# Kernel optimization log

Hardware: AMD Instinct MI355X
Metric: run time of the kernel (lower is better)

## Reference

```python
import jax, jax.numpy as jnp
import numpy as np
from jax import lax

EPS_COS = 1e-8  # torch F.cosine_similarity eps
EPS_GN = 1e-5   # torch GroupNorm eps


def setup_inputs() -> dict:
    key = jax.random.key(0)
    k1, k2, k3 = jax.random.split(key, 3)
    b, f, h, w = 4, 64, 64, 64
    fdm = jax.random.uniform(k1, (b, 1, 2 * h, 2 * w), dtype=jnp.float32)
    x = jax.random.normal(k2, (b, f, h, w), dtype=jnp.float32)
    W_fuse = jax.random.normal(k3, (f, 2 * f, 3, 3), dtype=jnp.float32) * 0.05
    b_fuse = jnp.zeros((f,), jnp.float32)
    gamma = jnp.ones((f,), jnp.float32)
    beta = jnp.zeros((f,), jnp.float32)
    return {"fdm": fdm, "x": x, "W_fuse": W_fuse, "b_fuse": b_fuse,
            "gamma": gamma, "beta": beta}


def reference(fdm, x, W_fuse, b_fuse, gamma, beta):
    b, f, h, w = x.shape
    # adaptive_max_pool2d(fdm, (h, w)): input spatial is exact multiple -> plain max pool
    kh, kw = fdm.shape[2] // h, fdm.shape[3] // w
    fdm_p = lax.reduce_window(fdm, -jnp.inf, lax.max,
                              (1, 1, kh, kw), (1, 1, kh, kw), 'VALID')  # [b,1,h,w]
    # per-sample threshold: min(0.5, max(fdm)/3)
    maxv = jnp.max(fdm_p, axis=(1, 2, 3))                 # [b]
    thre = jnp.minimum(0.5, maxv / 3.0)                   # [b]
    mask = fdm_p.reshape(b, h * w) >= thre[:, None]       # [b, HW] selected pixels

    # cosine similarity between selected feature vectors and all positions.
    # Original masked-selects N rows then computes N x HW sims and max-reduces over N;
    # we compute the full HW x HW sim and mask unselected rows to -inf (same max).
    xf = x.reshape(b, f, h * w).transpose(0, 2, 1)        # [b, HW, f]
    norm = jnp.sqrt(jnp.sum(xf * xf, axis=-1, keepdims=True))
    xn = xf / jnp.maximum(norm, EPS_COS)
    sim = jnp.einsum('bpf,bqf->bpq', xn, xn)              # [b, HW(sel), HW(all)]
    sim = jnp.where(mask[:, :, None], sim, -jnp.inf)
    sm = (jnp.max(sim, axis=1) / 2.0 + 0.5).reshape(b, 1, h, w)

    # fuse: Conv2d(2f -> f, k3, pad1) + GroupNorm(1, f) + ReLU
    cat = jnp.concatenate([sm * x, x], axis=1)            # [b, 2f, h, w]
    y = lax.conv_general_dilated(cat, W_fuse, (1, 1), 'SAME',
                                 dimension_numbers=('NCHW', 'OIHW', 'NCHW'))
    y = y + b_fuse[None, :, None, None]
    mu = jnp.mean(y, axis=(1, 2, 3), keepdims=True)
    var = jnp.mean((y - mu) ** 2, axis=(1, 2, 3), keepdims=True)
    y = (y - mu) / jnp.sqrt(var + EPS_GN)
    y = y * gamma[None, :, None, None] + beta[None, :, None, None]
    x0 = jax.nn.relu(y)
    return x0, sm
```

## Files before the change

kernel.cpp:

```cpp
#include <hip/hip_runtime.h>
#include <math.h>


#define HW 4096
#define NCH 64

typedef __attribute__((ext_vector_type(8))) short short8;
typedef __attribute__((ext_vector_type(4))) float f32x4;

static __device__ __forceinline__ ushort f2bf(float f) {
    unsigned u = __float_as_uint(f);
    unsigned r = (u + 0x7fffu + ((u >> 16) & 1u)) >> 16;
    return (ushort)r;
}
static __device__ __forceinline__ float bf2f(ushort h) {
    return __uint_as_float(((unsigned)h) << 16);
}
static __device__ __forceinline__ unsigned mapf(float f) {
    unsigned u = __float_as_uint(f);
    return u ^ ((unsigned)((int)u >> 31) | 0x80000000u);
}
static __device__ __forceinline__ float unmapf(unsigned u) {
    unsigned b = (u & 0x80000000u) ? (u ^ 0x80000000u) : ~u;
    return __uint_as_float(b);
}

__global__ __launch_bounds__(256) void k_pnp(
    const float* __restrict__ fdm, const float* __restrict__ x, const float* __restrict__ W,
    float* __restrict__ pooledOut, float* __restrict__ threOut,
    int* __restrict__ unsel, int* __restrict__ unselN, unsigned* __restrict__ scores,
    float* __restrict__ gnS1, float* __restrict__ gnS2,
    float* __restrict__ rn, float* __restrict__ smOut, ushort* __restrict__ inb,
    ushort* __restrict__ wbh, ushort* __restrict__ wbl) {
    const int t = threadIdx.x;
    if (blockIdx.x < 4) {
        const int b = blockIdx.x;
        __shared__ float pooled[4096];
        __shared__ float red[256];
        __shared__ int cnt;
        const float* fb = fdm + b * 16384;
        float lmax = -1.0f;
#pragma unroll
        for (int it = 0; it < 8; ++it) {
            int id2 = it * 256 + t;
            int i = id2 >> 5;
            int j2 = id2 & 31;
            const float* base = fb + i * 256 + j2 * 4;
            float4 a = *(const float4*)base;
            float4 c = *(const float4*)(base + 128);
            float p0 = fmaxf(fmaxf(a.x, a.y), fmaxf(c.x, c.y));
            float p1 = fmaxf(fmaxf(a.z, a.w), fmaxf(c.z, c.w));
            pooled[i * 64 + j2 * 2]     = p0;
            pooled[i * 64 + j2 * 2 + 1] = p1;
            lmax = fmaxf(lmax, fmaxf(p0, p1));
        }
        red[t] = lmax;
        __syncthreads();
        for (int s = 128; s > 0; s >>= 1) {
            if (t < s) red[t] = fmaxf(red[t], red[t + s]);
            __syncthreads();
        }
        __shared__ float thre_s;
        if (t == 0) {
            thre_s = fminf(0.5f, red[0] / 3.0f);
            cnt = 0;
            gnS1[b] = 0.0f; gnS2[b] = 0.0f;
        }
        __syncthreads();
        const float th = thre_s;
#pragma unroll
        for (int it = 0; it < 4; ++it) {
            int idx = (it * 256 + t) * 4;
            *(float4*)(pooledOut + b * 4096 + idx) = *(const float4*)(pooled + idx);
        }
        for (int idx = t; idx < 4096; idx += 256) {
            scores[b * 4096 + idx] = 0u;
            if (!(pooled[idx] >= th)) {
                int pos = atomicAdd(&cnt, 1);
                unsel[b * 4096 + pos] = idx;
            }
        }
        __syncthreads();
        if (t == 0) { unselN[b] = cnt; threOut[b] = th; }
    } else if (blockIdx.x < 260) {
        __shared__ float s_part[4][64];
        const int n = blockIdx.x - 4;
        const int b = n >> 6;
        const int pbase = (n & 63) * 64;
        const int wv = t >> 6;
        const int l = t & 63;
        const int sp = pbase + l;
        const float* xp = x + b * (NCH * HW) + sp;
        float xv[16];
        float ss = 0.f;
#pragma unroll
        for (int i = 0; i < 16; ++i) {
            float a = xp[(wv * 16 + i) * HW];
            xv[i] = a;
            ss += a * a;
        }
        s_part[wv][l] = ss;
        ushort h[16];
#pragma unroll
        for (int i = 0; i < 16; ++i) h[i] = f2bf(xv[i]);
        size_t dst1 = ((size_t)(b * 8 + wv) * 4096 + sp) * 16;
        size_t dst2 = ((size_t)(b * 8 + 4 + wv) * 4096 + sp) * 16;
        *(uint4*)(inb + dst1)     = *(const uint4*)h;
        *(uint4*)(inb + dst1 + 8) = *(const uint4*)(h + 8);
        *(uint4*)(inb + dst2)     = *(const uint4*)h;
        *(uint4*)(inb + dst2 + 8) = *(const uint4*)(h + 8);
        __syncthreads();
        if (t < 64) {
            float s = s_part[0][l] + s_part[1][l] + s_part[2][l] + s_part[3][l];
            int g = b * HW + pbase + l;
            rn[g] = 1.0f / fmaxf(sqrtf(s), 1e-8f);
            smOut[g] = 1.0f;
        }
    } else {
        const int u = (blockIdx.x - 260) * 256 + t;
        const int tap = u >> 10;
        const int rem = u & 1023;
        const int oc = rem >> 4;
        const int g = rem & 15;
        ushort hh[8], ll[8];
#pragma unroll
        for (int j = 0; j < 8; ++j) {
            int ic = g * 8 + j;
            float v = W[(oc * 128 + ic) * 9 + tap];
            ushort hb = f2bf(v);
            hh[j] = hb;
            ll[j] = f2bf(v - bf2f(hb));
        }
        *(uint4*)(wbh + (size_t)u * 8) = *(const uint4*)hh;
        *(uint4*)(wbl + (size_t)u * 8) = *(const uint4*)ll;
    }
}

__global__ __launch_bounds__(256) void k_score(
    const float* __restrict__ rn, const float* __restrict__ pooledM, const float* __restrict__ threArr,
    const int* __restrict__ unsel, const int* __restrict__ unselN,
    const ushort* __restrict__ inb, unsigned* __restrict__ scores) {
    const int b = blockIdx.y;
    const int n0 = blockIdx.x * 128;
    const int t = threadIdx.x;
    const int lane = t & 63;
    const int wave = t >> 6;
    const int li = lane & 15;
    const int quad = lane >> 4;
    const int nu = unselN[b];
    if (nu == 0) return;

    __shared__ __align__(16) ushort s_qh[64 * 72];
    __shared__ __align__(16) ushort s_ql[64 * 72];
    __shared__ unsigned s_best[64];

    const float th = threArr[b];
    const int p0 = n0 + (2 * wave) * 16 + li;
    const int p1 = n0 + (2 * wave + 1) * 16 + li;
    const float rp0 = rn[b * 4096 + p0];
    const float rp1 = rn[b * 4096 + p1];
    const float ng0 = (pooledM[b * 4096 + p0] >= th) ? 0.0f : -INFINITY;
    const float ng1 = (pooledM[b * 4096 + p1] >= th) ? 0.0f : -INFINITY;

    for (int qs0 = 0; qs0 < nu; qs0 += 64) {
        __syncthreads();
        for (int idx = t; idx < 512; idx += 256) {
            int q_l = idx >> 3;
            int part = idx & 7;
            int qg = qs0 + q_l;
            int q = 0;
            float rq = 0.0f;
            if (qg < nu) {
                q = unsel[b * 4096 + qg];
                rq = rn[b * 4096 + q];
            }
            uint4 raw = *(const uint4*)(inb + (((size_t)(b * 8 + 4 + (part >> 1)) * 4096) + q) * 16 + (part & 1) * 8);
            ushort hv[8]; *(uint4*)hv = raw;
            ushort hh[8], ll[8];
#pragma unroll
            for (int j = 0; j < 8; ++j) {
                float v = bf2f(hv[j]) * rq;
                hh[j] = f2bf(v);
                ll[j] = f2bf(v - bf2f(hh[j]));
            }
            int c0 = (part >> 1) * 16 + (part & 1) * 8;
            *(uint4*)(s_qh + q_l * 72 + c0) = *(const uint4*)hh;
            *(uint4*)(s_ql + q_l * 72 + c0) = *(const uint4*)ll;
        }
        if (t < 64) s_best[t] = 0u;
        __syncthreads();

        f32x4 acc[2][4];
#pragma unroll
        for (int nt = 0; nt < 2; ++nt)
#pragma unroll
            for (int mt = 0; mt < 4; ++mt) acc[nt][mt] = (f32x4){0.f, 0.f, 0.f, 0.f};
#pragma unroll
        for (int k0 = 0; k0 < 2; ++k0) {
            const int cb = k0 * 32 + quad * 8;
            const int grp = 4 + (cb >> 4);
            const int sub = cb & 15;
            short8 b0 = *(const short8*)(inb + (((size_t)(b * 8 + grp) * 4096) + p0) * 16 + sub);
            short8 b1 = *(const short8*)(inb + (((size_t)(b * 8 + grp) * 4096) + p1) * 16 + sub);
#pragma unroll
            for (int mt = 0; mt < 4; ++mt) {
                short8 ah = *(const short8*)(s_qh + (size_t)(mt * 16 + li) * 72 + cb);
                short8 al = *(const short8*)(s_ql + (size_t)(mt * 16 + li) * 72 + cb);
                acc[0][mt] = __builtin_amdgcn_mfma_f32_16x16x32_bf16(ah, b0, acc[0][mt], 0, 0, 0);
                acc[0][mt] = __builtin_amdgcn_mfma_f32_16x16x32_bf16(al, b0, acc[0][mt], 0, 0, 0);
                acc[1][mt] = __builtin_amdgcn_mfma_f32_16x16x32_bf16(ah, b1, acc[1][mt], 0, 0, 0);
                acc[1][mt] = __builtin_amdgcn_mfma_f32_16x16x32_bf16(al, b1, acc[1][mt], 0, 0, 0);
            }
        }
#pragma unroll
        for (int mt = 0; mt < 4; ++mt) {
#pragma unroll
            for (int r = 0; r < 4; ++r) {
                float sc = fmaxf(acc[0][mt][r] * rp0 + ng0, acc[1][mt][r] * rp1 + ng1);
                sc = fmaxf(sc, __shfl_xor(sc, 1));
                sc = fmaxf(sc, __shfl_xor(sc, 2));
                sc = fmaxf(sc, __shfl_xor(sc, 4));
                sc = fmaxf(sc, __shfl_xor(sc, 8));
                if (li == 0) atomicMax(&s_best[mt * 16 + quad * 4 + r], mapf(sc));
            }
        }
        __syncthreads();
        if (t < 64 && qs0 + t < nu) atomicMax(scores + b * 4096 + qs0 + t, s_best[t]);
    }
}

__global__ __launch_bounds__(256) void k_conv_mfma(
    const ushort* __restrict__ inb, const ushort* __restrict__ wbh, const ushort* __restrict__ wbl,
    const float* __restrict__ bfuse, const int* __restrict__ unsel, const int* __restrict__ unselN,
    const unsigned* __restrict__ scores, float* __restrict__ smOut,
    float* __restrict__ y, float* __restrict__ gnS1, float* __restrict__ gnS2) {
    const int rowblk = blockIdx.x;
    const int ocblk = blockIdx.y;
    const int b = blockIdx.z;
    const int t = threadIdx.x;
    const int lane = t & 63;
    const int wave = t >> 6;
    const int li = lane & 15;
    const int quad = lane >> 4;
    const int h0 = rowblk * 4;
    const int oc0 = ocblk * 16;
    const int nu = unselN[b];

    __shared__ __align__(16) ushort s_in[6 * 66 * 40];
    __shared__ __align__(16) ushort s_wh[9 * 16 * 40];
    __shared__ __align__(16) ushort s_wl[9 * 16 * 40];
    __shared__ float red1[256];
    __shared__ float red2[256];

    if (rowblk == 0 && ocblk == 0) {
        for (int qi = t; qi < nu; qi += 256) {
            float sm = unmapf(scores[b * 4096 + qi]) * 0.5f + 0.5f;
            smOut[b * 4096 + unsel[b * 4096 + qi]] = sm;
        }
    }

    f32x4 acc[4];
#pragma unroll
    for (int j = 0; j < 4; ++j) acc[j] = (f32x4){0.f, 0.f, 0.f, 0.f};

    for (int chunk = 0; chunk < 4; ++chunk) {
        __syncthreads();
        for (int idx = t; idx < 1584; idx += 256) {
            int part = idx & 3;
            int cell = idx >> 2;
            int r = cell / 66;
            int c = cell - r * 66;
            int h = h0 + r - 1;
            int w = c - 1;
            uint4 v = make_uint4(0u, 0u, 0u, 0u);
            if ((unsigned)h < 64u && (unsigned)w < 64u) {
                int grp = 2 * chunk + (part >> 1);
                int sub = part & 1;
                v = *(const uint4*)(inb + (((size_t)(b * 8 + grp) * 4096 + h * 64 + w) * 16 + sub * 8));
            }
            *(uint4*)(s_in + (size_t)cell * 40 + part * 8) = v;
        }
        const int ic0 = chunk * 32;
        for (int idx = t; idx < 1152; idx += 256) {
            int part = idx & 3;
            int uu = idx >> 2;
            int hl = uu / 144;
            int rem = uu - hl * 144;
            int tap = rem >> 4;
            int o = rem & 15;
            const ushort* src = (hl ? wbl : wbh) + ((size_t)(tap * 64 + oc0 + o) * 128 + ic0 + part * 8);
            uint4 v = *(const uint4*)src;
            ushort* dst = (hl ? s_wl : s_wh) + ((size_t)(tap * 16 + o) * 40 + part * 8);
            *(uint4*)dst = v;
        }
        if (chunk < 2) {
            __syncthreads();
            for (int idx = t; idx < nu * 4; idx += 256) {
                int qi = idx >> 2;
                int part = idx & 3;
                int q = unsel[b * 4096 + qi];
                int hq = q >> 6, wq = q & 63;
                int r = hq - h0 + 1;
                if ((unsigned)r < 6u) {
                    float sm = unmapf(scores[b * 4096 + qi]) * 0.5f + 0.5f;
                    ushort* ptr = s_in + (size_t)(r * 66 + wq + 1) * 40 + part * 8;
                    ushort hv[8];
                    *(uint4*)hv = *(const uint4*)ptr;
#pragma unroll
                    for (int j = 0; j < 8; ++j) hv[j] = f2bf(bf2f(hv[j]) * sm);
                    *(uint4*)ptr = *(const uint4*)hv;
                }
            }
        }
        __syncthreads();
#pragma unroll
        for (int kh = 0; kh < 3; ++kh) {
            const int r = wave + kh;
#pragma unroll
            for (int kw = 0; kw < 3; ++kw) {
                const int tap = kh * 3 + kw;
                short8 ah = *(const short8*)(s_wh + (size_t)(tap * 16 + li) * 40 + quad * 8);
                short8 al = *(const short8*)(s_wl + (size_t)(tap * 16 + li) * 40 + quad * 8);
#pragma unroll
                for (int j = 0; j < 4; ++j) {
                    int c = j * 16 + li + kw;
                    short8 bv = *(const short8*)(s_in + ((size_t)(r * 66 + c) * 40 + quad * 8));
                    acc[j] = __builtin_amdgcn_mfma_f32_16x16x32_bf16(ah, bv, acc[j], 0, 0, 0);
                    acc[j] = __builtin_amdgcn_mfma_f32_16x16x32_bf16(al, bv, acc[j], 0, 0, 0);
                }
            }
        }
    }
    float bias[4];
#pragma unroll
    for (int reg = 0; reg < 4; ++reg) bias[reg] = bfuse[oc0 + quad * 4 + reg];
    float s1 = 0.f, s2 = 0.f;
    const int hrow = h0 + wave;
#pragma unroll
    for (int j = 0; j < 4; ++j) {
#pragma unroll
        for (int reg = 0; reg < 4; ++reg) {
            float v = acc[j][reg] + bias[reg];
            y[((size_t)(b * 64 + oc0 + quad * 4 + reg)) * HW + hrow * 64 + j * 16 + li] = v;
            s1 += v; s2 += v * v;
        }
    }
    red1[t] = s1; red2[t] = s2;
    __syncthreads();
    for (int s = 128; s > 0; s >>= 1) {
        if (t < s) { red1[t] += red1[t + s]; red2[t] += red2[t + s]; }
        __syncthreads();
    }
    if (t == 0) {
        atomicAdd(&gnS1[b], red1[0]);
        atomicAdd(&gnS2[b], red2[0]);
    }
}

__global__ void k_gn(float* __restrict__ out, const float* __restrict__ gnS1, const float* __restrict__ gnS2,
                     const float* __restrict__ gamma, const float* __restrict__ beta) {
    const int e = (blockIdx.x * 256 + threadIdx.x) * 4;
    const int b = e >> 18;
    const int c = (e >> 12) & 63;
    const float inv = 1.0f / 262144.0f;
    float mu = gnS1[b] * inv;
    float var = gnS2[b] * inv - mu * mu;
    float rs = rsqrtf(var + 1e-5f);
    float scale = rs * gamma[c];
    float shift = beta[c] - mu * scale;
    float4 v = *(const float4*)(out + e);
    float4 o;
    o.x = fmaxf(v.x * scale + shift, 0.0f);
    o.y = fmaxf(v.y * scale + shift, 0.0f);
    o.z = fmaxf(v.z * scale + shift, 0.0f);
    o.w = fmaxf(v.w * scale + shift, 0.0f);
    *(float4*)(out + e) = o;
}

extern "C" void kernel_launch(void* const* d_in, const int* in_sizes, int n_in,
                              void* d_out, int out_size, void* d_ws, size_t ws_size,
                              hipStream_t stream) {
    const float* fdm   = (const float*)d_in[0];
    const float* x     = (const float*)d_in[1];
    const float* Wf    = (const float*)d_in[2];
    const float* bfuse = (const float*)d_in[3];
    const float* gamma = (const float*)d_in[4];
    const float* beta  = (const float*)d_in[5];
    float* out = (float*)d_out;
    float* ws  = (float*)d_ws;

    float*    rn      = ws;
    float*    pooledM = rn + 16384;
    int*      unsel   = (int*)(pooledM + 16384);
    unsigned* scores  = (unsigned*)(unsel + 16384);
    float*    thre    = (float*)(scores + 16384);
    int*      unselN  = (int*)(thre + 4);
    float*    gnS1    = (float*)(unselN + 4);
    float*    gnS2    = gnS1 + 4;
    ushort*   wbh     = (ushort*)(gnS2 + 4);
    ushort*   wbl     = wbh + 73728;
    ushort*   inb     = wbl + 73728;

    float* yout  = out;
    float* smOut = out + 1048576;

    k_pnp<<<dim3(296), dim3(256), 0, stream>>>(fdm, x, Wf, pooledM, thre, unsel, unselN,
                                               scores, gnS1, gnS2, rn, smOut, inb, wbh, wbl);
    k_score<<<dim3(32, 4), dim3(256), 0, stream>>>(rn, pooledM, thre, unsel, unselN, inb, scores);
    k_conv_mfma<<<dim3(16, 4, 4), dim3(256), 0, stream>>>(inb, wbh, wbl, bfuse, unsel, unselN,
                                                          scores, smOut, yout, gnS1, gnS2);
    k_gn<<<dim3(1024), dim3(256), 0, stream>>>(yout, gnS1, gnS2, gamma, beta);
}
```

Baseline: 106.9 us.

## Double-buffer conv input/weight staging with direct global-to-LDS async loads

Replaces the register-staged copies of the input tile and weights into shared memory in the conv kernel with global_load_lds direct transfers. It double-buffers LDS so the next channel chunk is fetched while MFMAs run on the current one. The layout changes to a per-part planar arrangement, and a zeroed global page stands in as the source for padding cells. Chunks are processed in the order 2,3,0,1 so the sm-scaled chunks arrive after a prefetch. This doubles LDS use, which may cut occupancy, and the new layout may raise LDS bank conflicts.

```diff
diff --git a/kernel.cpp b/kernel.cpp
--- a/kernel.cpp
+++ b/kernel.cpp
@@ -23,6 +23,10 @@
 static __device__ __forceinline__ float unmapf(unsigned u) {
     unsigned b = (u & 0x80000000u) ? (u ^ 0x80000000u) : ~u;
     return __uint_as_float(b);
+}
+static __device__ __forceinline__ void gl2lds(const void* g, void* l) {
+    __builtin_amdgcn_global_load_lds((const __attribute__((address_space(1))) void*)g,
+                                     (__attribute__((address_space(3))) void*)l, 16, 0, 0);
 }
 
 __global__ __launch_bounds__(256) void k_pnp(
@@ -31,7 +35,7 @@
     int* __restrict__ unsel, int* __restrict__ unselN, unsigned* __restrict__ scores,
     float* __restrict__ gnS1, float* __restrict__ gnS2,
     float* __restrict__ rn, float* __restrict__ smOut, ushort* __restrict__ inb,
-    ushort* __restrict__ wbh, ushort* __restrict__ wbl) {
+    ushort* __restrict__ wbh, ushort* __restrict__ wbl, uint4* __restrict__ zpage) {
     const int t = threadIdx.x;
     if (blockIdx.x < 4) {
         const int b = blockIdx.x;
@@ -65,6 +69,7 @@
             thre_s = fminf(0.5f, red[0] / 3.0f);
             cnt = 0;
             gnS1[b] = 0.0f; gnS2[b] = 0.0f;
+            if (b == 0) *zpage = make_uint4(0u, 0u, 0u, 0u);
         }
         __syncthreads();
         const float th = thre_s;
@@ -232,7 +237,7 @@
 __global__ __launch_bounds__(256) void k_conv_mfma(
     const ushort* __restrict__ inb, const ushort* __restrict__ wbh, const ushort* __restrict__ wbl,
     const float* __restrict__ bfuse, const int* __restrict__ unsel, const int* __restrict__ unselN,
-    const unsigned* __restrict__ scores, float* __restrict__ smOut,
+    const unsigned* __restrict__ scores, float* __restrict__ smOut, const uint4* __restrict__ zpage,
     float* __restrict__ y, float* __restrict__ gnS1, float* __restrict__ gnS2) {
     const int rowblk = blockIdx.x;
     const int ocblk = blockIdx.y;
@@ -246,9 +251,8 @@
     const int oc0 = ocblk * 16;
     const int nu = unselN[b];
 
-    __shared__ __align__(16) ushort s_in[6 * 66 * 40];
-    __shared__ __align__(16) ushort s_wh[9 * 16 * 40];
-    __shared__ __align__(16) ushort s_wl[9 * 16 * 40];
+    __shared__ __align__(16) ushort s_in[2][4 * 396 * 8];
+    __shared__ __align__(16) ushort s_w[2][4 * 288 * 8];
     __shared__ float red1[256];
     __shared__ float red2[256];
 
@@ -263,38 +267,48 @@
 #pragma unroll
     for (int j = 0; j < 4; ++j) acc[j] = (f32x4){0.f, 0.f, 0.f, 0.f};
 
-    for (int chunk = 0; chunk < 4; ++chunk) {
-        __syncthreads();
-        for (int idx = t; idx < 1584; idx += 256) {
-            int part = idx & 3;
-            int cell = idx >> 2;
-            int r = cell / 66;
-            int c = cell - r * 66;
-            int h = h0 + r - 1;
-            int w = c - 1;
-            uint4 v = make_uint4(0u, 0u, 0u, 0u);
-            if ((unsigned)h < 64u && (unsigned)w < 64u) {
-                int grp = 2 * chunk + (part >> 1);
-                int sub = part & 1;
-                v = *(const uint4*)(inb + (((size_t)(b * 8 + grp) * 4096 + h * 64 + w) * 16 + sub * 8));
-            }
-            *(uint4*)(s_in + (size_t)cell * 40 + part * 8) = v;
+    auto issue = [&](int chunk, int buf) {
+        const int part = wave;
+        const int grp = 2 * chunk + (part >> 1);
+        const int sub = (part & 1) * 8;
+        const ushort* gbase = inb + (((size_t)(b * 8 + grp)) * 4096) * 16 + sub;
+        ushort* lin = &s_in[buf][part * 3168];
+#pragma unroll
+        for (int i = 0; i < 7; ++i) {
+            int cell = i * 64 + lane;
+            if (cell < 396) {
+                int r = cell / 66;
+                int c = cell - r * 66;
+                int h = h0 + r - 1;
+                int w = c - 1;
+                bool ok = ((unsigned)h < 64u) && ((unsigned)w < 64u);
+                const void* src = ok ? (const void*)(gbase + (size_t)(h * 64 + w) * 16) : (const void*)zpage;
+                gl2lds(src, lin + i * 512);
+            }
         }
         const int ic0 = chunk * 32;
-        for (int idx = t; idx < 1152; idx += 256) {
-            int part = idx & 3;
-            int uu = idx >> 2;
-            int hl = uu / 144;
-            int rem = uu - hl * 144;
-            int tap = rem >> 4;
-            int o = rem & 15;
-            const ushort* src = (hl ? wbl : wbh) + ((size_t)(tap * 64 + oc0 + o) * 128 + ic0 + part * 8);
-            uint4 v = *(const uint4*)src;
-            ushort* dst = (hl ? s_wl : s_wh) + ((size_t)(tap * 16 + o) * 40 + part * 8);
-            *(uint4*)dst = v;
-        }
+        ushort* lw = &s_w[buf][part * 2304];
+#pragma unroll
+        for (int i = 0; i < 5; ++i) {
+            int j = i * 64 + lane;
+            if (j < 288) {
+                int hl = (j >= 144);
+                int e = j - hl * 144;
+                int tap = e >> 4;
+                int o = e & 15;
+                const ushort* src = (hl ? wbl : wbh) + ((size_t)(tap * 64 + oc0 + o) * 128 + ic0 + part * 8);
+                gl2lds(src, lw + i * 512);
+            }
+        }
+    };
+
+    issue(2, 0);
+
+    for (int a = 0; a < 4; ++a) {
+        const int chunk = a ^ 2;
+        const int buf = a & 1;
+        __syncthreads();
         if (chunk < 2) {
-            __syncthreads();
             for (int idx = t; idx < nu * 4; idx += 256) {
                 int qi = idx >> 2;
                 int part = idx & 3;
@@ -303,7 +317,7 @@
                 int r = hq - h0 + 1;
                 if ((unsigned)r < 6u) {
                     float sm = unmapf(scores[b * 4096 + qi]) * 0.5f + 0.5f;
-                    ushort* ptr = s_in + (size_t)(r * 66 + wq + 1) * 40 + part * 8;
+                    ushort* ptr = &s_in[buf][part * 3168 + (r * 66 + wq + 1) * 8];
                     ushort hv[8];
                     *(uint4*)hv = *(const uint4*)ptr;
 #pragma unroll
@@ -311,22 +325,27 @@
                     *(uint4*)ptr = *(const uint4*)hv;
                 }
             }
-        }
-        __syncthreads();
-#pragma unroll
-        for (int kh = 0; kh < 3; ++kh) {
-            const int r = wave + kh;
-#pragma unroll
-            for (int kw = 0; kw < 3; ++kw) {
-                const int tap = kh * 3 + kw;
-                short8 ah = *(const short8*)(s_wh + (size_t)(tap * 16 + li) * 40 + quad * 8);
-                short8 al = *(const short8*)(s_wl + (size_t)(tap * 16 + li) * 40 + quad * 8);
-#pragma unroll
-                for (int j = 0; j < 4; ++j) {
-                    int c = j * 16 + li + kw;
-                    short8 bv = *(const short8*)(s_in + ((size_t)(r * 66 + c) * 40 + quad * 8));
-                    acc[j] = __builtin_amdgcn_mfma_f32_16x16x32_bf16(ah, bv, acc[j], 0, 0, 0);
-                    acc[j] = __builtin_amdgcn_mfma_f32_16x16x32_bf16(al, bv, acc[j], 0, 0, 0);
+            __syncthreads();
+        }
+        if (a < 3) issue((a + 1) ^ 2, 1 - buf);
+        {
+            const ushort* sin = &s_in[buf][quad * 3168];
+            const ushort* swq = &s_w[buf][quad * 2304];
+#pragma unroll
+            for (int kh = 0; kh < 3; ++kh) {
+                const int r = wave + kh;
+#pragma unroll
+                for (int kw = 0; kw < 3; ++kw) {
+                    const int tap = kh * 3 + kw;
+                    short8 ah = *(const short8*)(swq + (tap * 16 + li) * 8);
+                    short8 al = *(const short8*)(swq + 1152 + (tap * 16 + li) * 8);
+#pragma unroll
+                    for (int j = 0; j < 4; ++j) {
+                        int c = j * 16 + li + kw;
+                        short8 bv = *(const short8*)(sin + (r * 66 + c) * 8);
+                        acc[j] = __builtin_amdgcn_mfma_f32_16x16x32_bf16(ah, bv, acc[j], 0, 0, 0);
+                        acc[j] = __builtin_amdgcn_mfma_f32_16x16x32_bf16(al, bv, acc[j], 0, 0, 0);
+                    }
                 }
             }
         }
@@ -397,7 +416,8 @@
     int*      unselN  = (int*)(thre + 4);
     float*    gnS1    = (float*)(unselN + 4);
     float*    gnS2    = gnS1 + 4;
-    ushort*   wbh     = (ushort*)(gnS2 + 4);
+    uint4*    zpage   = (uint4*)(gnS2 + 4);
+    ushort*   wbh     = (ushort*)(zpage + 1);
     ushort*   wbl     = wbh + 73728;
     ushort*   inb     = wbl + 73728;
 
@@ -405,9 +425,9 @@
     float* smOut = out + 1048576;
 
     k_pnp<<<dim3(296), dim3(256), 0, stream>>>(fdm, x, Wf, pooledM, thre, unsel, unselN,
-                                               scores, gnS1, gnS2, rn, smOut, inb, wbh, wbl);
+                                               scores, gnS1, gnS2, rn, smOut, inb, wbh, wbl, zpage);
     k_score<<<dim3(32, 4), dim3(256), 0, stream>>>(rn, pooledM, thre, unsel, unselN, inb, scores);
     k_conv_mfma<<<dim3(16, 4, 4), dim3(256), 0, stream>>>(inb, wbh, wbl, bfuse, unsel, unselN,
-                                                          scores, smOut, yout, gnS1, gnS2);
+                                                          scores, smOut, zpage, yout, gnS1, gnS2);
     k_gn<<<dim3(1024), dim3(256), 0, stream>>>(yout, gnS1, gnS2, gamma, beta);
 }
```

Result: faster. 99.98 us (median of 2 runs) (-6.4%).
